# Performance work log

Measured on AMD Instinct MI355X. Metric: run time of the kernel, lower is better.

Reference implementation:

```python
import jax, jax.numpy as jnp
import numpy as np

N, E, H, C, L = 10000, 320000, 4, 128, 4  # nodes, edges, heads, hidden, gat layers
D_IN, E_DIM = 7, 5


def setup_inputs() -> dict:
    key = jax.random.key(0)
    ks = jax.random.split(key, 16)
    g = lambda i, shape, s=0.05: jax.random.normal(ks[i], shape, dtype=jnp.float32) * s
    z = lambda *s: jnp.zeros(s, jnp.float32)
    o = lambda *s: jnp.ones(s, jnp.float32)
    return {
        "x": g(0, (N, D_IN), 1.0),
        "edge_index": jax.random.randint(ks[1], (2, E), 0, N),
        "edge_attr": g(2, (E, E_DIM), 1.0),
        "emb_W": g(3, (D_IN, C)), "emb_b": z(C),
        "gat_Wl": g(4, (L, C, H * C)), "gat_Wr": g(5, (L, C, H * C)),
        "gat_We": g(6, (L, E_DIM, H * C)), "gat_att": g(7, (L, H, C)),
        "gat_b": z(L, C), "ln_g": o(L, C), "ln_b": z(L, C),
        "sp_W1": g(8, (2 * C, C)), "sp_b1": z(C),
        "sp_W2": g(9, (C, C)), "sp_b2": z(C),
        "sp_gW": g(10, (C, C)), "sp_gb": z(C),
        "fn_g": o(C), "fn_b": z(C),
    }


def _layernorm(x, g, b, eps=1e-5):
    m = x.mean(-1, keepdims=True)
    v = ((x - m) ** 2).mean(-1, keepdims=True)
    return (x - m) * jax.lax.rsqrt(v + eps) * g + b


def _gatv2(h, src, dst, edge_attr, Wl, Wr, We, att, b):
    # GATv2Conv(concat=False, edge_dim): x_j = Wl h[src], x_i = Wr h[dst]
    xl = (h @ Wl).reshape(-1, H, C)            # [N,H,C]
    xr = (h @ Wr).reshape(-1, H, C)            # [N,H,C]
    e = (edge_attr @ We).reshape(-1, H, C)      # [E,H,C]
    m = jax.nn.leaky_relu(xl[src] + xr[dst] + e, 0.2)
    logits = jnp.einsum('ehc,hc->eh', m, att)   # [E,H]
    mx = jax.ops.segment_max(logits, dst, num_segments=N)
    ex = jnp.exp(logits - mx[dst])
    den = jax.ops.segment_sum(ex, dst, num_segments=N)
    alpha = ex / den[dst]                       # softmax over incoming edges
    out = jax.ops.segment_sum(alpha[..., None] * xl[src], dst, num_segments=N)
    return out.mean(axis=1) + b                 # head-average (concat=False)


def _social_pool(h, src, dst, W1, b1, W2, b2, gW, gb):
    pair = jnp.concatenate([h[src], h[dst]], axis=-1)   # [E,2C]
    inter = jax.nn.relu(pair @ W1 + b1) @ W2 + b2       # [E,C]
    gated = inter * jax.nn.sigmoid(inter @ gW + gb)
    s = jax.ops.segment_sum(gated, src, num_segments=N)
    cnt = jax.ops.segment_sum(jnp.ones((src.shape[0],), h.dtype), src, num_segments=N)
    return s / jnp.maximum(cnt, 1.0)[:, None]           # scatter-mean


def reference(x, edge_index, edge_attr, emb_W, emb_b, gat_Wl, gat_Wr, gat_We,
              gat_att, gat_b, ln_g, ln_b, sp_W1, sp_b1, sp_W2, sp_b2,
              sp_gW, sp_gb, fn_g, fn_b):
    src, dst = edge_index[0], edge_index[1]
    h = jax.nn.relu(x @ emb_W + emb_b)
    for i in range(L):
        res = h
        h = _gatv2(h, src, dst, edge_attr, gat_Wl[i], gat_Wr[i], gat_We[i],
                   gat_att[i], gat_b[i])
        h = jax.nn.relu(h)
        h = _layernorm(h + res, ln_g[i], ln_b[i])
    h = h + _social_pool(h, src, dst, sp_W1, sp_b1, sp_W2, sp_b2, sp_gW, sp_gb)
    return _layernorm(h, fn_g, fn_b)
```

## Files before the change

kernel.cpp:

```cpp
#include <hip/hip_runtime.h>
#include <hip/hip_bf16.h>
#include <math.h>

#define N_NODES 10000
#define N_EDGES 320000
#define HEADS   4
#define CDIM    128
#define HC      512
#define LAYERS  4
#define DIN     7
#define EDIM    5

typedef short short8 __attribute__((ext_vector_type(8)));
typedef unsigned short us8 __attribute__((ext_vector_type(8)));
typedef float f32x4 __attribute__((ext_vector_type(4)));

__device__ __forceinline__ void atomAddF(float* p, float v) { unsafeAtomicAdd(p, v); }

__device__ __forceinline__ unsigned short f2bf(float f) {
  unsigned u = __float_as_uint(f);
  unsigned r = u + 0x7fffu + ((u >> 16) & 1u);
  return (unsigned short)(r >> 16);
}
__device__ __forceinline__ float bf2f(unsigned short u) {
  return __uint_as_float(((unsigned)u) << 16);
}

__global__ __launch_bounds__(256) void embed_kernel(
    const float* __restrict__ x, const float* __restrict__ W,
    const float* __restrict__ b, float* __restrict__ h, unsigned short* __restrict__ hbf)
{
  int t = blockIdx.x * 256 + threadIdx.x;
  int n = t >> 7, c = t & 127;
  float acc = b[c];
#pragma unroll
  for (int k = 0; k < DIN; ++k) acc += x[n * DIN + k] * W[k * CDIM + c];
  acc = fmaxf(acc, 0.f);
  h[t] = acc;
  hbf[t] = f2bf(acc);
}

__global__ __launch_bounds__(256) void pack_kernel(
    const float* __restrict__ Wl, const float* __restrict__ Wr,
    const float* __restrict__ W1, const float* __restrict__ W2,
    const float* __restrict__ gW, unsigned short* __restrict__ WlrT,
    unsigned short* __restrict__ W1T, unsigned short* __restrict__ W2T,
    unsigned short* __restrict__ gWT, unsigned short* __restrict__ W2bf)
{
  int t = blockIdx.x * 256 + threadIdx.x;
  if (t < 524288) {
    int k = t & 127, n = (t >> 7) & 1023, l = t >> 17;
    float v = (n < 512) ? Wl[(size_t)(l * 128 + k) * 512 + n]
                        : Wr[(size_t)(l * 128 + k) * 512 + (n - 512)];
    WlrT[t] = f2bf(v);
  } else if (t < 524288 + 32768) {
    int u = t - 524288; int k = u & 127, n = u >> 7;
    float v = (n < 128) ? W1[k * 128 + n] : W1[(128 + k) * 128 + (n - 128)];
    W1T[u] = f2bf(v);
  } else if (t < 557056 + 16384) {
    int u = t - 557056; int k = u & 127, n = u >> 7;
    W2T[u] = f2bf(W2[k * 128 + n]);
  } else if (t < 573440 + 16384) {
    int u = t - 573440; int k = u & 127, n = u >> 7;
    gWT[u] = f2bf(gW[k * 128 + n]);
  } else if (t < 589824 + 16384) {
    int u = t - 589824;
    W2bf[u] = f2bf(W2[u]);
  }
}

__global__ __launch_bounds__(128) void fuse_bias_kernel(
    const float* __restrict__ b2, const float* __restrict__ gW,
    const float* __restrict__ gb, float* __restrict__ gbF)
{
  int n = threadIdx.x;
  float s = gb[n];
  for (int k = 0; k < 128; ++k) s += b2[k] * gW[k * 128 + n];
  gbF[n] = s;
}

__global__ __launch_bounds__(256) void hist_kernel(
    const int* __restrict__ ei, int* __restrict__ degD, int* __restrict__ degS)
{
  int e = blockIdx.x * 256 + threadIdx.x;
  if (e < N_EDGES) {
    atomicAdd(&degS[ei[e]], 1);
    atomicAdd(&degD[ei[N_EDGES + e]], 1);
  }
}

__global__ __launch_bounds__(1024) void scan_kernel(
    const int* __restrict__ degD, int* __restrict__ offD, int* __restrict__ curD,
    const int* __restrict__ degS, int* __restrict__ offS, int* __restrict__ curS, int n)
{
  __shared__ int wsum[16];
  __shared__ int carry;
  int tid = threadIdx.x, wid = tid >> 6, lane = tid & 63;
  for (int arr = 0; arr < 2; ++arr) {
    const int* deg = arr ? degS : degD;
    int* off = arr ? offS : offD;
    int* cur = arr ? curS : curD;
    if (tid == 0) carry = 0;
    __syncthreads();
    for (int base = 0; base < n; base += 1024) {
      int i = base + tid;
      int v = (i < n) ? deg[i] : 0;
      int incl = v;
#pragma unroll
      for (int o = 1; o < 64; o <<= 1) {
        int t2 = __shfl_up(incl, o);
        if (lane >= o) incl += t2;
      }
      if (lane == 63) wsum[wid] = incl;
      __syncthreads();
      if (tid < 16) {
        int wv = wsum[tid];
#pragma unroll
        for (int o = 1; o < 16; o <<= 1) {
          int t2 = __shfl_up(wv, o);
          if (tid >= o) wv += t2;
        }
        wsum[tid] = wv;
      }
      __syncthreads();
      int woff = (wid > 0) ? wsum[wid - 1] : 0;
      int excl = carry + woff + incl - v;
      if (i < n) { off[i] = excl; cur[i] = excl; }
      __syncthreads();
      if (tid == 0) carry += wsum[15];
      __syncthreads();
    }
    if (tid == 0) off[n] = carry;
    __syncthreads();
  }
}

__global__ __launch_bounds__(256) void scatter_kernel(
    const int* __restrict__ ei, int* __restrict__ curD, int* __restrict__ curS,
    int* __restrict__ eidD, int* __restrict__ eidS)
{
  int e = blockIdx.x * 256 + threadIdx.x;
  if (e < N_EDGES) {
    int s = ei[e], d = ei[N_EDGES + e];
    int p = atomicAdd(&curD[d], 1);
    eidD[p] = e;
    int q = atomicAdd(&curS[s], 1);
    eidS[q] = e;
  }
}

__global__ __launch_bounds__(256) void reorder_kernel(
    const int* __restrict__ ei, const float* __restrict__ eattr,
    const int* __restrict__ eidD, int* __restrict__ esrc,
    float4* __restrict__ ea4, float* __restrict__ ea1)
{
  int idx = blockIdx.x * 256 + threadIdx.x;
  if (idx < N_EDGES) {
    int e = eidD[idx];
    esrc[idx] = ei[e];
    const float* p = &eattr[(size_t)e * 5];
    ea4[idx] = make_float4(p[0], p[1], p[2], p[3]);
    ea1[idx] = p[4];
  } else if (idx < N_EDGES + 16) {
    esrc[idx] = 0;
    ea4[idx] = make_float4(0.f, 0.f, 0.f, 0.f);
    ea1[idx] = 0.f;
  }
}

__global__ __launch_bounds__(256) void mfma_gemm_kernel(
    const unsigned short* __restrict__ A, const unsigned short* __restrict__ BT,
    unsigned short* __restrict__ C, int M, int ldc)
{
  __shared__ __align__(16) unsigned short sA[64 * 128];
  __shared__ __align__(16) unsigned short sB[64 * 128];
  int tid = threadIdx.x;
  int bm = blockIdx.y * 64, bn = blockIdx.x * 64;
#pragma unroll
  for (int i = 0; i < 4; ++i) {
    int ch = tid + i * 256;
    int r = ch >> 4, kc = ch & 15;
    int gr = bm + r;
    short8 v = {0, 0, 0, 0, 0, 0, 0, 0};
    if (gr < M) v = *(const short8*)&A[(size_t)gr * 128 + kc * 8];
    *(short8*)&sA[r * 128 + ((kc ^ (r & 7)) * 8)] = v;
  }
#pragma unroll
  for (int i = 0; i < 4; ++i) {
    int ch = tid + i * 256;
    int r = ch >> 4, kc = ch & 15;
    short8 v = *(const short8*)&BT[(size_t)(bn + r) * 128 + kc * 8];
    *(short8*)&sB[r * 128 + ((kc ^ (r & 7)) * 8)] = v;
  }
  __syncthreads();
  int w = tid >> 6, lane = tid & 63;
  int wr = (w >> 1) * 32, wc = (w & 1) * 32;
  int l15 = lane & 15, q = lane >> 4;
  f32x4 acc00 = {0, 0, 0, 0}, acc01 = acc00, acc10 = acc00, acc11 = acc00;
#pragma unroll
  for (int ks = 0; ks < 4; ++ks) {
    int c0 = ks * 4 + q;
    int m0 = wr + l15, m1 = m0 + 16;
    int n0 = wc + l15, n1 = n0 + 16;
    short8 a0 = *(const short8*)&sA[m0 * 128 + ((c0 ^ (m0 & 7)) * 8)];
    short8 a1 = *(const short8*)&sA[m1 * 128 + ((c0 ^ (m1 & 7)) * 8)];
    short8 b0 = *(const short8*)&sB[n0 * 128 + ((c0 ^ (n0 & 7)) * 8)];
    short8 b1 = *(const short8*)&sB[n1 * 128 + ((c0 ^ (n1 & 7)) * 8)];
    acc00 = __builtin_amdgcn_mfma_f32_16x16x32_bf16(a0, b0, acc00, 0, 0, 0);
    acc01 = __builtin_amdgcn_mfma_f32_16x16x32_bf16(a0, b1, acc01, 0, 0, 0);
    acc10 = __builtin_amdgcn_mfma_f32_16x16x32_bf16(a1, b0, acc10, 0, 0, 0);
    acc11 = __builtin_amdgcn_mfma_f32_16x16x32_bf16(a1, b1, acc11, 0, 0, 0);
  }
#pragma unroll
  for (int mf = 0; mf < 2; ++mf) {
#pragma unroll
    for (int nf = 0; nf < 2; ++nf) {
      f32x4 acc = mf == 0 ? (nf == 0 ? acc00 : acc01) : (nf == 0 ? acc10 : acc11);
      int col = bn + wc + nf * 16 + l15;
#pragma unroll
      for (int r = 0; r < 4; ++r) {
        int row = bm + wr + mf * 16 + 4 * q + r;
        if (row < M) C[(size_t)row * ldc + col] = f2bf(acc[r]);
      }
    }
  }
}

__global__ __launch_bounds__(256) void gat_agg_kernel(
    const float* __restrict__ h_in, float* __restrict__ h_out,
    unsigned short* __restrict__ hbf_out, const unsigned short* __restrict__ xlr,
    const int* __restrict__ esrc, const float4* __restrict__ ea4,
    const float* __restrict__ ea1, const int* __restrict__ offD,
    const float* __restrict__ We, const float* __restrict__ att,
    const float* __restrict__ gbias, const float* __restrict__ lng,
    const float* __restrict__ lnb)
{
  int tid = threadIdx.x;
  int w = tid >> 6, lane = tid & 63;
  int n = blockIdx.x * 4 + w;
  int base = lane * 8;

  float wWe[5][8];
#pragma unroll
  for (int k = 0; k < 5; ++k) {
    float4 a = *(const float4*)&We[k * HC + base];
    float4 b = *(const float4*)&We[k * HC + base + 4];
    wWe[k][0] = a.x; wWe[k][1] = a.y; wWe[k][2] = a.z; wWe[k][3] = a.w;
    wWe[k][4] = b.x; wWe[k][5] = b.y; wWe[k][6] = b.z; wWe[k][7] = b.w;
  }
  float wAtt[8];
  {
    float4 a = *(const float4*)&att[base];
    float4 b = *(const float4*)&att[base + 4];
    wAtt[0] = a.x; wAtt[1] = a.y; wAtt[2] = a.z; wAtt[3] = a.w;
    wAtt[4] = b.x; wAtt[5] = b.y; wAtt[6] = b.z; wAtt[7] = b.w;
  }
  float xr_reg[8];
  {
    us8 u = *(const us8*)&xlr[(size_t)n * 1024 + 512 + base];
#pragma unroll
    for (int j = 0; j < 8; ++j) xr_reg[j] = bf2f(u[j]);
  }

  int e0 = offD[n], e1 = offD[n + 1];
  float dsum = 0.f;
  float acc[8] = {0.f, 0.f, 0.f, 0.f, 0.f, 0.f, 0.f, 0.f};

  if (e0 < e1) {
    us8 uA = *(const us8*)&xlr[(size_t)esrc[e0    ] * 1024 + base];
    us8 uB = *(const us8*)&xlr[(size_t)esrc[e0 + 1] * 1024 + base];
    us8 uC = *(const us8*)&xlr[(size_t)esrc[e0 + 2] * 1024 + base];
    us8 uD = *(const us8*)&xlr[(size_t)esrc[e0 + 3] * 1024 + base];
    float4 qaA = ea4[e0];     float qeA = ea1[e0];
    float4 qaB = ea4[e0 + 1]; float qeB = ea1[e0 + 1];
    int sN0 = esrc[e0 + 4], sN1 = esrc[e0 + 5];

    for (int i = e0; i < e1; i += 4) {
      float x0[8], x1[8];
#pragma unroll
      for (int j = 0; j < 8; ++j) { x0[j] = bf2f(uA[j]); x1[j] = bf2f(uB[j]); }
      uA = *(const us8*)&xlr[(size_t)sN0 * 1024 + base];
      uB = *(const us8*)&xlr[(size_t)sN1 * 1024 + base];
      float4 qaC = ea4[i + 2]; float qeC = ea1[i + 2];
      float4 qaD = ea4[i + 3]; float qeD = ea1[i + 3];
      int sN2 = esrc[i + 6], sN3 = esrc[i + 7];

      float lg0 = 0.f, lg1 = 0.f;
#pragma unroll
      for (int j = 0; j < 8; ++j) {
        float v0 = x0[j] + xr_reg[j] + qaA.x * wWe[0][j] + qaA.y * wWe[1][j]
                 + qaA.z * wWe[2][j] + qaA.w * wWe[3][j] + qeA * wWe[4][j];
        lg0 += fmaxf(v0, 0.2f * v0) * wAtt[j];
        float v1 = x1[j] + xr_reg[j] + qaB.x * wWe[0][j] + qaB.y * wWe[1][j]
                 + qaB.z * wWe[2][j] + qaB.w * wWe[3][j] + qeB * wWe[4][j];
        lg1 += fmaxf(v1, 0.2f * v1) * wAtt[j];
      }
      lg0 += __shfl_xor(lg0, 1); lg1 += __shfl_xor(lg1, 1);
      lg0 += __shfl_xor(lg0, 2); lg1 += __shfl_xor(lg1, 2);
      lg0 += __shfl_xor(lg0, 4); lg1 += __shfl_xor(lg1, 4);
      lg0 += __shfl_xor(lg0, 8); lg1 += __shfl_xor(lg1, 8);
      lg1 = (i + 1 < e1) ? lg1 : -INFINITY;
      {
        float p0 = __expf(lg0);
        float p1 = __expf(lg1);
        dsum += p0 + p1;
#pragma unroll
        for (int j = 0; j < 8; ++j)
          acc[j] = fmaf(p1, x1[j], fmaf(p0, x0[j], acc[j]));
      }

      float x2[8], x3[8];
#pragma unroll
      for (int j = 0; j < 8; ++j) { x2[j] = bf2f(uC[j]); x3[j] = bf2f(uD[j]); }
      uC = *(const us8*)&xlr[(size_t)sN2 * 1024 + base];
      uD = *(const us8*)&xlr[(size_t)sN3 * 1024 + base];
      qaA = ea4[i + 4]; qeA = ea1[i + 4];
      qaB = ea4[i + 5]; qeB = ea1[i + 5];
      sN0 = esrc[i + 8]; sN1 = esrc[i + 9];

      float lg2 = 0.f, lg3 = 0.f;
#pragma unroll
      for (int j = 0; j < 8; ++j) {
        float v2 = x2[j] + xr_reg[j] + qaC.x * wWe[0][j] + qaC.y * wWe[1][j]
                 + qaC.z * wWe[2][j] + qaC.w * wWe[3][j] + qeC * wWe[4][j];
        lg2 += fmaxf(v2, 0.2f * v2) * wAtt[j];
        float v3 = x3[j] + xr_reg[j] + qaD.x * wWe[0][j] + qaD.y * wWe[1][j]
                 + qaD.z * wWe[2][j] + qaD.w * wWe[3][j] + qeD * wWe[4][j];
        lg3 += fmaxf(v3, 0.2f * v3) * wAtt[j];
      }
      lg2 += __shfl_xor(lg2, 1); lg3 += __shfl_xor(lg3, 1);
      lg2 += __shfl_xor(lg2, 2); lg3 += __shfl_xor(lg3, 2);
      lg2 += __shfl_xor(lg2, 4); lg3 += __shfl_xor(lg3, 4);
      lg2 += __shfl_xor(lg2, 8); lg3 += __shfl_xor(lg3, 8);
      lg2 = (i + 2 < e1) ? lg2 : -INFINITY;
      lg3 = (i + 3 < e1) ? lg3 : -INFINITY;
      {
        float p2 = __expf(lg2);
        float p3 = __expf(lg3);
        dsum += p2 + p3;
#pragma unroll
        for (int j = 0; j < 8; ++j)
          acc[j] = fmaf(p3, x3[j], fmaf(p2, x2[j], acc[j]));
      }
    }
  }

  float inv = (dsum > 0.f) ? (1.f / dsum) : 0.f;
  int c8 = (lane & 15) * 8;
  float o[8];
  float s1 = 0.f, s2 = 0.f;
#pragma unroll
  for (int j = 0; j < 8; ++j) {
    float v = acc[j] * inv;
    v += __shfl_xor(v, 16);
    v += __shfl_xor(v, 32);
    float oo = 0.25f * v + gbias[c8 + j];
    oo = fmaxf(oo, 0.f);
    oo += h_in[(size_t)n * 128 + c8 + j];
    o[j] = oo;
    s1 += oo; s2 += oo * oo;
  }
  s1 += __shfl_xor(s1, 1);  s2 += __shfl_xor(s2, 1);
  s1 += __shfl_xor(s1, 2);  s2 += __shfl_xor(s2, 2);
  s1 += __shfl_xor(s1, 4);  s2 += __shfl_xor(s2, 4);
  s1 += __shfl_xor(s1, 8);  s2 += __shfl_xor(s2, 8);
  s1 += __shfl_xor(s1, 16); s2 += __shfl_xor(s2, 16);
  s1 += __shfl_xor(s1, 32); s2 += __shfl_xor(s2, 32);
  float mean = s1 * (1.f / 512.f);
  float var = s2 * (1.f / 512.f) - mean * mean;
  float rs = rsqrtf(var + 1e-5f);
  if (lane < 16) {
#pragma unroll
    for (int j = 0; j < 8; ++j) {
      float val = (o[j] - mean) * rs * lng[c8 + j] + lnb[c8 + j];
      h_out[(size_t)n * 128 + c8 + j] = val;
      hbf_out[(size_t)n * 128 + c8 + j] = f2bf(val);
    }
  }
}

__global__ __launch_bounds__(512) void sp_edge_kernel(
    const unsigned short* __restrict__ sab, const float* __restrict__ b1,
    const unsigned short* __restrict__ W2T, const float* __restrict__ b2,
    const unsigned short* __restrict__ FT, const float* __restrict__ gbF,
    const int* __restrict__ ei, const int* __restrict__ eidS,
    float* __restrict__ pool)
{
  __shared__ __align__(16) float gT[128 * 65];
  __shared__ int rsrc[64];
  __shared__ int rdst[64];
  unsigned short* sT = (unsigned short*)gT;
  int tid = threadIdx.x;
  int w = tid >> 6, lane = tid & 63;
  int l15 = lane & 15, q = lane >> 4;
  int col = w * 16 + l15;

  short8 bW[4], bF[4];
#pragma unroll
  for (int ks = 0; ks < 4; ++ks) {
    bW[ks] = *(const short8*)&W2T[(size_t)col * 128 + (ks * 4 + q) * 8];
    bF[ks] = *(const short8*)&FT [(size_t)col * 128 + (ks * 4 + q) * 8];
  }
  float b2c = b2[col];
  float gbc = gbF[col];

  int ebase = blockIdx.x * 64;
  if (tid < 64) {
    int e = eidS[ebase + tid];
    rsrc[tid] = ei[e];
    rdst[tid] = ei[N_EDGES + e];
  }
  __syncthreads();

#pragma unroll
  for (int i = 0; i < 2; ++i) {
    int ch = tid + i * 512;
    int r = ch >> 4, kc = ch & 15, c0 = kc * 8;
    int s = rsrc[r], d = rdst[r];
    us8 ua = *(const us8*)&sab[(size_t)s * 256 + c0];
    us8 ub = *(const us8*)&sab[(size_t)d * 256 + 128 + c0];
    float4 bb0 = *(const float4*)&b1[c0];
    float4 bb1 = *(const float4*)&b1[c0 + 4];
    float bv[8] = {bb0.x, bb0.y, bb0.z, bb0.w, bb1.x, bb1.y, bb1.z, bb1.w};
    short8 o;
#pragma unroll
    for (int j = 0; j < 8; ++j)
      o[j] = (short)f2bf(fmaxf(bf2f(ua[j]) + bf2f(ub[j]) + bv[j], 0.f));
    *(short8*)&sT[r * 128 + ((kc ^ (r & 7)) * 8)] = o;
  }
  __syncthreads();

  f32x4 acc1[4], acc2[4];
#pragma unroll
  for (int rg = 0; rg < 4; ++rg) {
    int mr = rg * 16 + l15;
    acc1[rg] = (f32x4){0, 0, 0, 0};
    acc2[rg] = (f32x4){0, 0, 0, 0};
#pragma unroll
    for (int ks = 0; ks < 4; ++ks) {
      short8 a = *(const short8*)&sT[mr * 128 + (((ks * 4 + q) ^ (mr & 7)) * 8)];
      acc1[rg] = __builtin_amdgcn_mfma_f32_16x16x32_bf16(a, bW[ks], acc1[rg], 0, 0, 0);
      acc2[rg] = __builtin_amdgcn_mfma_f32_16x16x32_bf16(a, bF[ks], acc2[rg], 0, 0, 0);
    }
  }
  __syncthreads();

#pragma unroll
  for (int rg = 0; rg < 4; ++rg) {
    int rb = rg * 16 + 4 * q;
#pragma unroll
    for (int r = 0; r < 4; ++r) {
      float inter = acc1[rg][r] + b2c;
      float gg = acc2[rg][r] + gbc;
      gT[col * 65 + rb + r] = inter * (1.f / (1.f + __expf(-gg)));
    }
  }
  __syncthreads();

  if (tid < 256) {
    int c = tid & 127, half = tid >> 7;
    int rbeg = half * 32, rend = rbeg + 32;
    int curs = -1; float run = 0.f;
    for (int r = rbeg; r < rend; ++r) {
      int s = rsrc[r];
      if (s != curs) {
        if (curs >= 0) atomAddF(&pool[(size_t)curs * 128 + c], run);
        curs = s; run = 0.f;
      }
      run += gT[c * 65 + r];
    }
    atomAddF(&pool[(size_t)curs * 128 + c], run);
  }
}

__global__ __launch_bounds__(256) void finalize_kernel(
    const float* __restrict__ h, const float* __restrict__ pool,
    const int* __restrict__ degS, const float* __restrict__ g,
    const float* __restrict__ b, float* __restrict__ out)
{
  int t = blockIdx.x * 256 + threadIdx.x;
  int n = t >> 6, lane = t & 63;
  if (n >= N_NODES) return;
  float cnt = fmaxf((float)degS[n], 1.f);
  float a = h[(size_t)n * 128 + lane] + pool[(size_t)n * 128 + lane] / cnt;
  float c2 = h[(size_t)n * 128 + 64 + lane] + pool[(size_t)n * 128 + 64 + lane] / cnt;
  float s = a + c2, s2 = a * a + c2 * c2;
#pragma unroll
  for (int o = 1; o < 64; o <<= 1) { s += __shfl_xor(s, o); s2 += __shfl_xor(s2, o); }
  float mean = s * (1.f / 128.f);
  float var = s2 * (1.f / 128.f) - mean * mean;
  float rs = rsqrtf(var + 1e-5f);
  out[(size_t)n * 128 + lane] = (a - mean) * rs * g[lane] + b[lane];
  out[(size_t)n * 128 + 64 + lane] = (c2 - mean) * rs * g[64 + lane] + b[64 + lane];
}

extern "C" void kernel_launch(void* const* d_in, const int* in_sizes, int n_in,
                              void* d_out, int out_size, void* d_ws, size_t ws_size,
                              hipStream_t stream) {
  (void)in_sizes; (void)n_in; (void)out_size; (void)ws_size;
  const float* x     = (const float*)d_in[0];
  const int*   ei    = (const int*)d_in[1];
  const float* eattr = (const float*)d_in[2];
  const float* embW  = (const float*)d_in[3];
  const float* embB  = (const float*)d_in[4];
  const float* gWl   = (const float*)d_in[5];
  const float* gWr   = (const float*)d_in[6];
  const float* gWe   = (const float*)d_in[7];
  const float* gAtt  = (const float*)d_in[8];
  const float* gB    = (const float*)d_in[9];
  const float* lnG   = (const float*)d_in[10];
  const float* lnB   = (const float*)d_in[11];
  const float* spW1  = (const float*)d_in[12];
  const float* spB1  = (const float*)d_in[13];
  const float* spW2  = (const float*)d_in[14];
  const float* spB2  = (const float*)d_in[15];
  const float* spGW  = (const float*)d_in[16];
  const float* spGB  = (const float*)d_in[17];
  const float* fnG   = (const float*)d_in[18];
  const float* fnB   = (const float*)d_in[19];
  float* out = (float*)d_out;

  char* ws = (char*)d_ws;
  size_t off = 0;
  auto alloc = [&](size_t bytes) {
    void* p = ws + off;
    off = (off + bytes + 255) & ~(size_t)255;
    return p;
  };
  float* hA   = (float*)alloc((size_t)N_NODES * 128 * 4);
  float* hB   = (float*)alloc((size_t)N_NODES * 128 * 4);
  unsigned short* hbfA = (unsigned short*)alloc((size_t)N_NODES * 128 * 2);
  unsigned short* hbfB = (unsigned short*)alloc((size_t)N_NODES * 128 * 2);
  unsigned short* xlr  = (unsigned short*)alloc((size_t)N_NODES * 1024 * 2);
  unsigned short* sab  = (unsigned short*)alloc((size_t)N_NODES * 256 * 2);
  float* pool = (float*)alloc((size_t)N_NODES * 128 * 4);
  unsigned short* WlrT = (unsigned short*)alloc((size_t)4 * 1024 * 128 * 2);
  unsigned short* W1T  = (unsigned short*)alloc((size_t)256 * 128 * 2);
  unsigned short* W2T  = (unsigned short*)alloc((size_t)128 * 128 * 2);
  unsigned short* gWT  = (unsigned short*)alloc((size_t)128 * 128 * 2);
  unsigned short* W2bf = (unsigned short*)alloc((size_t)128 * 128 * 2);
  unsigned short* FT   = (unsigned short*)alloc((size_t)128 * 128 * 2);
  float* gbF = (float*)alloc((size_t)128 * 4);
  int* degD = (int*)alloc((size_t)N_NODES * 4);
  int* degS = (int*)alloc((size_t)N_NODES * 4);
  int* offD = (int*)alloc((size_t)(N_NODES + 1) * 4);
  int* offS = (int*)alloc((size_t)(N_NODES + 1) * 4);
  int* curD = (int*)alloc((size_t)N_NODES * 4);
  int* curS = (int*)alloc((size_t)N_NODES * 4);
  int* eidD = (int*)alloc((size_t)N_EDGES * 4);
  int* eidS = (int*)alloc((size_t)N_EDGES * 4);
  int* esrc = (int*)alloc((size_t)(N_EDGES + 16) * 4);
  float4* ea4 = (float4*)alloc((size_t)(N_EDGES + 16) * 16);
  float* ea1 = (float*)alloc((size_t)(N_EDGES + 16) * 4);

  hipMemsetAsync(degD, 0, (size_t)N_NODES * 4, stream);
  hipMemsetAsync(degS, 0, (size_t)N_NODES * 4, stream);
  hipMemsetAsync(pool, 0, (size_t)N_NODES * 128 * 4, stream);

  pack_kernel<<<(606208 + 255) / 256, 256, 0, stream>>>(gWl, gWr, spW1, spW2, spGW,
                                                        WlrT, W1T, W2T, gWT, W2bf);
  mfma_gemm_kernel<<<dim3(2, 2), 256, 0, stream>>>(gWT, W2bf, FT, 128, 128);
  fuse_bias_kernel<<<1, 128, 0, stream>>>(spB2, spGW, spGB, gbF);

  embed_kernel<<<(N_NODES * 128) / 256, 256, 0, stream>>>(x, embW, embB, hA, hbfA);
  hist_kernel<<<(N_EDGES + 255) / 256, 256, 0, stream>>>(ei, degD, degS);
  scan_kernel<<<1, 1024, 0, stream>>>(degD, offD, curD, degS, offS, curS, N_NODES);
  scatter_kernel<<<(N_EDGES + 255) / 256, 256, 0, stream>>>(ei, curD, curS, eidD, eidS);
  reorder_kernel<<<(N_EDGES + 16 + 255) / 256, 256, 0, stream>>>(ei, eattr, eidD, esrc, ea4, ea1);

  const int MB64 = (N_NODES + 63) / 64;
  float* hcur = hA; float* hnext = hB;
  unsigned short* hbcur = hbfA; unsigned short* hbnext = hbfB;
  for (int l = 0; l < LAYERS; ++l) {
    mfma_gemm_kernel<<<dim3(16, MB64), 256, 0, stream>>>(
        hbcur, WlrT + (size_t)l * 1024 * 128, xlr, N_NODES, 1024);
    gat_agg_kernel<<<(N_NODES + 3) / 4, 256, 0, stream>>>(hcur, hnext, hbnext, xlr,
                                                          esrc, ea4, ea1, offD,
                                                          gWe + (size_t)l * EDIM * HC,
                                                          gAtt + (size_t)l * HC,
                                                          gB + (size_t)l * 128,
                                                          lnG + (size_t)l * 128,
                                                          lnB + (size_t)l * 128);
    float* t1 = hcur; hcur = hnext; hnext = t1;
    unsigned short* t2 = hbcur; hbcur = hbnext; hbnext = t2;
  }
  mfma_gemm_kernel<<<dim3(4, MB64), 256, 0, stream>>>(hbcur, W1T, sab, N_NODES, 256);
  sp_edge_kernel<<<N_EDGES / 64, 512, 0, stream>>>(sab, spB1, W2T, spB2, FT, gbF,
                                                   ei, eidS, pool);
  finalize_kernel<<<(N_NODES + 3) / 4, 256, 0, stream>>>(hcur, pool, degS, fnG, fnB, out);
}
```

Baseline: 798.1 us.

## Split each node's incoming-edge aggregation across two wavefronts and reduce through LDS

Each destination node's edge range is now split in half between two wavefronts, and the grid is doubled so there are two nodes per block instead of four. The partial accumulators and softmax denominators are combined through shared memory, after which one wavefront runs the epilogue. This targets latency-bound gathers on high-degree nodes by putting more wavefronts in flight per node. In exchange it adds an LDS round trip, a block barrier, and duplicated per-wave loads of weights and xr, and half the wavefronts sit idle during the epilogue. Because it drops the max subtraction and relies on plain exp, partial sums combine without rescaling, as before.

```diff
diff --git a/kernel.cpp b/kernel.cpp
--- a/kernel.cpp
+++ b/kernel.cpp
@@ -235,9 +235,12 @@
     const float* __restrict__ gbias, const float* __restrict__ lng,
     const float* __restrict__ lnb)
 {
+  __shared__ float sAcc[4][64][8];
+  __shared__ float sDsum[4][64];
   int tid = threadIdx.x;
   int w = tid >> 6, lane = tid & 63;
-  int n = blockIdx.x * 4 + w;
+  int n = blockIdx.x * 2 + (w >> 1);
+  int half = w & 1;
   int base = lane * 8;
 
   float wWe[5][8];
@@ -263,19 +266,23 @@
   }
 
   int e0 = offD[n], e1 = offD[n + 1];
+  int mid = e0 + ((e1 - e0 + 1) >> 1);
+  int b0 = half ? mid : e0;
+  int b1 = half ? e1 : mid;
+
   float dsum = 0.f;
   float acc[8] = {0.f, 0.f, 0.f, 0.f, 0.f, 0.f, 0.f, 0.f};
 
-  if (e0 < e1) {
-    us8 uA = *(const us8*)&xlr[(size_t)esrc[e0    ] * 1024 + base];
-    us8 uB = *(const us8*)&xlr[(size_t)esrc[e0 + 1] * 1024 + base];
-    us8 uC = *(const us8*)&xlr[(size_t)esrc[e0 + 2] * 1024 + base];
-    us8 uD = *(const us8*)&xlr[(size_t)esrc[e0 + 3] * 1024 + base];
-    float4 qaA = ea4[e0];     float qeA = ea1[e0];
-    float4 qaB = ea4[e0 + 1]; float qeB = ea1[e0 + 1];
-    int sN0 = esrc[e0 + 4], sN1 = esrc[e0 + 5];
-
-    for (int i = e0; i < e1; i += 4) {
+  if (b0 < b1) {
+    us8 uA = *(const us8*)&xlr[(size_t)esrc[b0    ] * 1024 + base];
+    us8 uB = *(const us8*)&xlr[(size_t)esrc[b0 + 1] * 1024 + base];
+    us8 uC = *(const us8*)&xlr[(size_t)esrc[b0 + 2] * 1024 + base];
+    us8 uD = *(const us8*)&xlr[(size_t)esrc[b0 + 3] * 1024 + base];
+    float4 qaA = ea4[b0];     float qeA = ea1[b0];
+    float4 qaB = ea4[b0 + 1]; float qeB = ea1[b0 + 1];
+    int sN0 = esrc[b0 + 4], sN1 = esrc[b0 + 5];
+
+    for (int i = b0; i < b1; i += 4) {
       float x0[8], x1[8];
 #pragma unroll
       for (int j = 0; j < 8; ++j) { x0[j] = bf2f(uA[j]); x1[j] = bf2f(uB[j]); }
@@ -299,7 +306,7 @@
       lg0 += __shfl_xor(lg0, 2); lg1 += __shfl_xor(lg1, 2);
       lg0 += __shfl_xor(lg0, 4); lg1 += __shfl_xor(lg1, 4);
       lg0 += __shfl_xor(lg0, 8); lg1 += __shfl_xor(lg1, 8);
-      lg1 = (i + 1 < e1) ? lg1 : -INFINITY;
+      lg1 = (i + 1 < b1) ? lg1 : -INFINITY;
       {
         float p0 = __expf(lg0);
         float p1 = __expf(lg1);
@@ -332,8 +339,8 @@
       lg2 += __shfl_xor(lg2, 2); lg3 += __shfl_xor(lg3, 2);
       lg2 += __shfl_xor(lg2, 4); lg3 += __shfl_xor(lg3, 4);
       lg2 += __shfl_xor(lg2, 8); lg3 += __shfl_xor(lg3, 8);
-      lg2 = (i + 2 < e1) ? lg2 : -INFINITY;
-      lg3 = (i + 3 < e1) ? lg3 : -INFINITY;
+      lg2 = (i + 2 < b1) ? lg2 : -INFINITY;
+      lg3 = (i + 3 < b1) ? lg3 : -INFINITY;
       {
         float p2 = __expf(lg2);
         float p3 = __expf(lg3);
@@ -344,6 +351,16 @@
       }
     }
   }
+
+#pragma unroll
+  for (int j = 0; j < 8; ++j) sAcc[w][lane][j] = acc[j];
+  sDsum[w][lane] = dsum;
+  __syncthreads();
+  if (half) return;
+
+#pragma unroll
+  for (int j = 0; j < 8; ++j) acc[j] += sAcc[w + 1][lane][j];
+  dsum += sDsum[w + 1][lane];
 
   float inv = (dsum > 0.f) ? (1.f / dsum) : 0.f;
   int c8 = (lane & 15) * 8;
@@ -574,13 +591,13 @@
   for (int l = 0; l < LAYERS; ++l) {
     mfma_gemm_kernel<<<dim3(16, MB64), 256, 0, stream>>>(
         hbcur, WlrT + (size_t)l * 1024 * 128, xlr, N_NODES, 1024);
-    gat_agg_kernel<<<(N_NODES + 3) / 4, 256, 0, stream>>>(hcur, hnext, hbnext, xlr,
-                                                          esrc, ea4, ea1, offD,
-                                                          gWe + (size_t)l * EDIM * HC,
-                                                          gAtt + (size_t)l * HC,
-                                                          gB + (size_t)l * 128,
-                                                          lnG + (size_t)l * 128,
-                                                          lnB + (size_t)l * 128);
+    gat_agg_kernel<<<N_NODES / 2, 256, 0, stream>>>(hcur, hnext, hbnext, xlr,
+                                                    esrc, ea4, ea1, offD,
+                                                    gWe + (size_t)l * EDIM * HC,
+                                                    gAtt + (size_t)l * HC,
+                                                    gB + (size_t)l * 128,
+                                                    lnG + (size_t)l * 128,
+                                                    lnB + (size_t)l * 128);
     float* t1 = hcur; hcur = hnext; hnext = t1;
     unsigned short* t2 = hbcur; hbcur = hbnext; hbnext = t2;
   }
```

Result: slower. 855.0 us (+7.1%).
